# Performance work log

Measured on AMD Instinct MI355X. Metric: run time of the kernel, lower is better.

The kernel has to match this reference:

```python
import jax, jax.numpy as jnp
import numpy as np
from jax import lax

WAY = 20
EPS = 1e-10
CE_EPS = 1e-7
BN_EPS = 1e-3


def _conv_block(x, k, b, g, be):
    # conv 3x3 SAME -> batchnorm (batch stats, training mode) -> relu -> maxpool 2x2
    x = lax.conv_general_dilated(x, k, (1, 1), 'SAME',
                                 dimension_numbers=('NHWC', 'HWIO', 'NHWC')) + b
    m = x.mean((0, 1, 2))
    v = x.var((0, 1, 2))
    x = (x - m) * lax.rsqrt(v + BN_EPS) * g + be
    x = jax.nn.relu(x)
    x = lax.reduce_window(x, -jnp.inf, lax.max, (1, 2, 2, 1), (1, 2, 2, 1), 'VALID')
    return x


def _embed(x, cps):
    for (k, b, g, be) in cps:
        x = _conv_block(x, k, b, g, be)
    return x.reshape(x.shape[0], -1)  # [B, 1600]


def _lstm(seq, Wx, Wh, b):
    # seq: [batch, time, feat] -> [batch, time, hidden]
    B = seq.shape[0]
    H = Wh.shape[0]
    def step(carry, xt):
        h, c = carry
        z = xt @ Wx + h @ Wh + b
        i, f, g, o = jnp.split(z, 4, axis=-1)
        c = jax.nn.sigmoid(f) * c + jax.nn.sigmoid(i) * jnp.tanh(g)
        h = jax.nn.sigmoid(o) * jnp.tanh(c)
        return (h, c), h
    init = (jnp.zeros((B, H), seq.dtype), jnp.zeros((B, H), seq.dtype))
    _, hs = lax.scan(step, init, jnp.swapaxes(seq, 0, 1))
    return jnp.swapaxes(hs, 0, 1)


def _bilstm(seq, fk, fr, fb, bk, br, bb):
    fwd = _lstm(seq, fk, fr, fb)
    bwd = _lstm(seq[:, ::-1], bk, br, bb)[:, ::-1]
    return jnp.concatenate([fwd, bwd], axis=-1)


def setup_inputs() -> dict:
    key = jax.random.key(0)
    ks = jax.random.split(key, 12)
    B, S, Q, H, W, C = 32, 20, 5, 84, 84, 3
    inp = {
        'x_support': jax.random.normal(ks[0], (B, S, H, W, C), jnp.float32),
        'y_support': jax.random.randint(ks[1], (B, S), 0, WAY, jnp.int32),
        'x_query': jax.random.normal(ks[2], (B, Q, H, W, C), jnp.float32),
        'y_query': jax.random.randint(ks[3], (B, Q), 0, WAY, jnp.int32),
        'k1': jax.random.normal(ks[4], (3, 3, 3, 64), jnp.float32) * 0.05,
        'b1': jnp.zeros((64,), jnp.float32), 'g1': jnp.ones((64,), jnp.float32), 'be1': jnp.zeros((64,), jnp.float32),
        'k2': jax.random.normal(ks[5], (3, 3, 64, 64), jnp.float32) * 0.05,
        'b2': jnp.zeros((64,), jnp.float32), 'g2': jnp.ones((64,), jnp.float32), 'be2': jnp.zeros((64,), jnp.float32),
        'k3': jax.random.normal(ks[6], (3, 3, 64, 64), jnp.float32) * 0.05,
        'b3': jnp.zeros((64,), jnp.float32), 'g3': jnp.ones((64,), jnp.float32), 'be3': jnp.zeros((64,), jnp.float32),
        'k4': jax.random.normal(ks[7], (3, 3, 64, 64), jnp.float32) * 0.05,
        'b4': jnp.zeros((64,), jnp.float32), 'g4': jnp.ones((64,), jnp.float32), 'be4': jnp.zeros((64,), jnp.float32),
        'fk': jax.random.normal(ks[8], (1600, 128), jnp.float32) * 0.05,
        'fr': jax.random.normal(ks[9], (32, 128), jnp.float32) * 0.05,
        'fb': jnp.zeros((128,), jnp.float32),
        'bk': jax.random.normal(ks[10], (1600, 128), jnp.float32) * 0.05,
        'br': jax.random.normal(ks[11], (32, 128), jnp.float32) * 0.05,
        'bb': jnp.zeros((128,), jnp.float32),
    }
    return inp


def reference(x_support, y_support, x_query, y_query,
              k1, b1, g1, be1, k2, b2, g2, be2, k3, b3, g3, be3, k4, b4, g4, be4,
              fk, fr, fb, bk, br, bb):
    cps = ((k1, b1, g1, be1), (k2, b2, g2, be2), (k3, b3, g3, be3), (k4, b4, g4, be4))
    B, S = x_support.shape[:2]
    Q = x_query.shape[1]

    # per-sample embedding (BN stats per slice, matching the original per-i g() calls)
    sup_emb = jax.vmap(lambda xs: _embed(xs, cps), in_axes=1)(x_support)  # [S, B, F]
    qry_emb = jax.vmap(lambda xs: _embed(xs, cps), in_axes=1)(x_query)    # [Q, B, F]

    # stack [support..., query] -> [S+1, B, F]; Keras LSTM treats axis0 as batch, axis1(=B) as time
    seqs = jnp.concatenate([jnp.broadcast_to(sup_emb[None], (Q,) + sup_emb.shape),
                            qry_emb[:, None]], axis=1)  # [Q, S+1, B, F]
    outs = jax.vmap(lambda s: _bilstm(s, fk, fr, fb, bk, br, bb))(seqs)  # [Q, S+1, B, 64]

    sup = outs[:, :-1]   # [Q, S, B, 64]
    qry = outs[:, -1]    # [Q, B, 64]

    # cosine distance: only the support vector is normalized (faithful to original)
    mag = lax.rsqrt(jnp.maximum(jnp.sum(sup * sup, axis=-1), EPS))  # [Q, S, B]
    dot = jnp.einsum('qbd,qsbd->qsb', qry, sup)                      # [Q, S, B]
    sim = jax.nn.softmax(jnp.transpose(dot * mag, (0, 2, 1)), axis=-1)  # [Q, B, S]

    y_sup_oh = jax.nn.one_hot(y_support, WAY, dtype=jnp.float32)    # [B, S, WAY]
    preds = jnp.einsum('qbs,bsw->qbw', sim, y_sup_oh)                # [Q, B, WAY]

    y_q_oh = jnp.transpose(jax.nn.one_hot(y_query, WAY, dtype=jnp.float32), (1, 0, 2))  # [Q, B, WAY]
    ce = -jnp.sum(y_q_oh * jnp.log(jnp.clip(preds, CE_EPS, 1.0 - CE_EPS)), axis=-1)      # [Q, B]
    ce_out = jnp.sum(ce, axis=0) / Q  # [B]

    pred_lbl = jnp.argmax(preds, axis=-1).astype(jnp.int32)          # [Q, B]
    eq = (pred_lbl == jnp.transpose(y_query).astype(jnp.int32)).astype(jnp.float32)
    acc = jnp.sum(jnp.mean(eq, axis=1)) / Q  # scalar
    return (ce_out, acc)
```

## Files before the change

kernel.cpp:

```cpp
#include <hip/hip_runtime.h>
#include <hip/hip_bf16.h>


#define NG 25
#define NI 32

typedef _Float16 half8v __attribute__((ext_vector_type(8)));
typedef __attribute__((ext_vector_type(4))) float float4v;

__device__ __forceinline__ unsigned short f2h(float f) {
    _Float16 h = (_Float16)f;
    union { _Float16 h; unsigned short u; } cv; cv.h = h;
    return cv.u;
}
__device__ __forceinline__ float h2f(unsigned short u) {
    union { unsigned short u; _Float16 h; } cv; cv.u = u;
    return (float)cv.h;
}

__device__ __forceinline__ float fsigm(float x) {
    return __builtin_amdgcn_rcpf(1.f + exp2f(-1.44269504f * x));
}
__device__ __forceinline__ float ftanh(float x) {
    return 1.f - 2.f * __builtin_amdgcn_rcpf(1.f + exp2f(2.88539008f * x));
}

__global__ __launch_bounds__(256)
void wcvt_kernel(const float* __restrict__ wk, unsigned short* __restrict__ w16t) {
    int tap = blockIdx.x;
    for (int e = threadIdx.x; e < 4096; e += 256) {
        int co = e >> 6, ci = e & 63;
        w16t[(size_t)tap * 4096 + e] = f2h(wk[(size_t)tap * 4096 + ci * 64 + co]);
    }
}

__global__ __launch_bounds__(256)
void conv3m_kernel(const float* __restrict__ xs, const float* __restrict__ xq,
                   const float* __restrict__ wk, unsigned short* __restrict__ pool1h,
                   float* __restrict__ part, int g0) {
    __shared__ _Float16 sIn[10][304];
    __shared__ float sred[4][2][64];
    int gi = blockIdx.x;
    int gl = gi >> 5, i = gi & 31;
    int g = g0 + gl;
    int band = blockIdx.y;
    const float* base = (g < 20) ? xs + (size_t)(i * 20 + g) * (84 * 84 * 3)
                                 : xq + (size_t)(i * 5 + (g - 20)) * (84 * 84 * 3);
    int r0 = band * 8;
    for (int p = threadIdx.x; p < 10 * 152; p += 256) {
        int rr = p / 152, ep = (p - rr * 152) * 2;
        int r = r0 - 1 + rr;
        float v0 = 0.f, v1 = 0.f;
        if (ep < 294 && (unsigned)r < 84u) {
            int col0 = ep / 3 - 1, ci0 = ep - (ep / 3) * 3;
            if ((unsigned)col0 < 84u) v0 = base[((size_t)r * 84 + col0) * 3 + ci0];
            int e1 = ep + 1;
            if (e1 < 294) {
                int col1 = e1 / 3 - 1, ci1 = e1 - (e1 / 3) * 3;
                if ((unsigned)col1 < 84u) v1 = base[((size_t)r * 84 + col1) * 3 + ci1];
            }
        }
        unsigned int pk = (unsigned int)f2h(v0) | ((unsigned int)f2h(v1) << 16);
        ((unsigned int*)&sIn[rr][0])[p - rr * 152] = pk;
    }
    int lane = threadIdx.x & 63;
    int wv = threadIdx.x >> 6;
    int gq = lane >> 4;
    int l16 = lane & 15;
    int rowo[8], eo[8]; bool kv[8];
    #pragma unroll
    for (int j = 0; j < 8; ++j) {
        int k = 8 * gq + j;
        kv[j] = (k < 27);
        int kk = kv[j] ? k : 0;
        int kh = kk / 9; int rem = kk - kh * 9; int kw = rem / 3; int ci = rem - kw * 3;
        rowo[j] = kv[j] ? kh : 0;
        eo[j] = kw * 3 + ci;
    }
    half8v bfr[4];
    #pragma unroll
    for (int ct = 0; ct < 4; ++ct)
        #pragma unroll
        for (int j = 0; j < 8; ++j) {
            int k = 8 * gq + j;
            float w = (k < 27) ? wk[(size_t)k * 64 + ct * 16 + l16] : 0.f;
            bfr[ct][j] = (_Float16)w;
        }
    __syncthreads();

    bool rowv = (r0 + 2 * wv) < 84;
    int prow = band * 4 + wv;
    int sr = 2 * wv;
    float sA[4] = {0.f, 0.f, 0.f, 0.f}, sB[4] = {0.f, 0.f, 0.f, 0.f};

    #pragma unroll 1
    for (int tile = 0; tile < 6; ++tile) {
        int c0 = tile * 16;
        int w = c0 + l16;
        int eoff[8];
        #pragma unroll
        for (int j = 0; j < 8; ++j) eoff[j] = kv[j] ? (w * 3 + eo[j]) : 294;
        float4v acc0[4], acc1[4];
        #pragma unroll
        for (int ct = 0; ct < 4; ++ct) {
            acc0[ct] = (float4v){0.f, 0.f, 0.f, 0.f};
            acc1[ct] = (float4v){0.f, 0.f, 0.f, 0.f};
        }
        #pragma unroll
        for (int rs = 0; rs < 2; ++rs) {
            half8v af;
            #pragma unroll
            for (int j = 0; j < 8; ++j)
                af[j] = sIn[sr + rs + rowo[j]][eoff[j]];
            if (rs == 0) {
                #pragma unroll
                for (int ct = 0; ct < 4; ++ct)
                    acc0[ct] = __builtin_amdgcn_mfma_f32_16x16x32_f16(af, bfr[ct], acc0[ct], 0, 0, 0);
            } else {
                #pragma unroll
                for (int ct = 0; ct < 4; ++ct)
                    acc1[ct] = __builtin_amdgcn_mfma_f32_16x16x32_f16(af, bfr[ct], acc1[ct], 0, 0, 0);
            }
        }
        #pragma unroll
        for (int ct = 0; ct < 4; ++ct) {
            #pragma unroll
            for (int r = 0; r < 4; ++r) {
                float a0 = acc0[ct][r], a1 = acc1[ct][r];
                sA[ct] += a0 + a1;
                sB[ct] = fmaf(a0, a0, fmaf(a1, a1, sB[ct]));
            }
            if (rowv) {
                float m01 = fmaxf(fmaxf(acc0[ct][0], acc0[ct][1]),
                                  fmaxf(acc1[ct][0], acc1[ct][1]));
                float m23 = fmaxf(fmaxf(acc0[ct][2], acc0[ct][3]),
                                  fmaxf(acc1[ct][2], acc1[ct][3]));
                int pc0 = (c0 + gq * 4) >> 1;
                size_t rowbase = (((size_t)gi * 42 + prow) * 42) * 64 + ct * 16 + l16;
                if (pc0 < 42)     pool1h[rowbase + (size_t)pc0 * 64] = f2h(m01);
                if (pc0 + 1 < 42) pool1h[rowbase + (size_t)(pc0 + 1) * 64] = f2h(m23);
            }
        }
    }
    #pragma unroll
    for (int ct = 0; ct < 4; ++ct) {
        float s = sA[ct], q = sB[ct];
        s += __shfl_xor(s, 16); s += __shfl_xor(s, 32);
        q += __shfl_xor(q, 16); q += __shfl_xor(q, 32);
        if (gq == 0) { sred[wv][0][ct * 16 + l16] = s; sred[wv][1][ct * 16 + l16] = q; }
    }
    __syncthreads();
    if (threadIdx.x < 64) {
        int co = threadIdx.x;
        float s = sred[0][0][co] + sred[1][0][co] + sred[2][0][co] + sred[3][0][co];
        float q = sred[0][1][co] + sred[1][1][co] + sred[2][1][co] + sred[3][1][co];
        size_t pr = (size_t)blockIdx.y * gridDim.x + blockIdx.x;
        part[pr * 128 + co] = s;
        part[pr * 128 + 64 + co] = q;
    }
}

template<int D>
__global__ __launch_bounds__(256)
void conv64m_kernel(const unsigned short* __restrict__ act16,
                    const unsigned short* __restrict__ w16t,
                    float* __restrict__ poolout, float* __restrict__ part) {
    constexpr int nCT = (D + 15) / 16;
    constexpr int PD = D / 2;
    __shared__ __align__(16) char smem[64 * 72 * 2 * 2];
    unsigned short (*Albs)[72] = (unsigned short(*)[72])smem;
    unsigned short (*Blbs)[72] = (unsigned short(*)[72])(smem + 64 * 72 * 2);
    float (*lds2)[68] = (float(*)[68])smem;
    __shared__ float redst[2][4][64];

    int gi = blockIdx.x;
    int rt = blockIdx.y / nCT, ctile = blockIdx.y % nCT;
    int r0 = rt * 8, c0 = ctile * 16;
    const unsigned short* in = act16 + (size_t)gi * D * D * 64;

    int lane = threadIdx.x & 63;
    int wv = threadIdx.x >> 6;
    int pw = wv * 16;

    int spos = threadIdx.x >> 2;
    int scig = threadIdx.x & 3;
    int str = spos >> 4, stc = spos & 15;
    int sh = r0 + str, swc = c0 + stc;
    bool pval = (sh < D) && (swc < D);

    float4v acc[4];
    #pragma unroll
    for (int ct = 0; ct < 4; ++ct) acc[ct] = (float4v){0.f, 0.f, 0.f, 0.f};

    #pragma unroll 1
    for (int tap = 0; tap < 9; ++tap) {
        int kh = tap / 3, kw = tap - kh * 3;
        int hi = sh + kh - 1, wi = swc + kw - 1;
        uint4 av0 = {0,0,0,0}, av1 = {0,0,0,0};
        if (pval && (unsigned)hi < (unsigned)D && (unsigned)wi < (unsigned)D) {
            const uint4* src = (const uint4*)(in + ((size_t)hi * D + wi) * 64 + scig * 16);
            av0 = src[0]; av1 = src[1];
        }
        const uint4* wsrc = (const uint4*)(w16t + ((size_t)tap * 64 + spos) * 64 + scig * 16);
        uint4 bv0 = wsrc[0], bv1 = wsrc[1];
        __syncthreads();
        *(uint4*)&Albs[spos][scig * 16]     = av0;
        *(uint4*)&Albs[spos][scig * 16 + 8] = av1;
        *(uint4*)&Blbs[spos][scig * 16]     = bv0;
        *(uint4*)&Blbs[spos][scig * 16 + 8] = bv1;
        __syncthreads();
        #pragma unroll
        for (int ks = 0; ks < 2; ++ks) {
            half8v afrag = *(const half8v*)&Albs[pw + (lane & 15)][ks * 32 + (lane >> 4) * 8];
            #pragma unroll
            for (int ct = 0; ct < 4; ++ct) {
                half8v bfrag = *(const half8v*)&Blbs[ct * 16 + (lane & 15)][ks * 32 + (lane >> 4) * 8];
                acc[ct] = __builtin_amdgcn_mfma_f32_16x16x32_f16(afrag, bfrag, acc[ct], 0, 0, 0);
            }
        }
    }

    __syncthreads();
    #pragma unroll
    for (int ct = 0; ct < 4; ++ct) {
        #pragma unroll
        for (int r = 0; r < 4; ++r) {
            int pos = pw + (lane >> 4) * 4 + r;
            int co = ct * 16 + (lane & 15);
            lds2[pos][co] = acc[ct][r];
        }
    }
    __syncthreads();
    {
        int co = threadIdx.x & 63;
        int p4 = threadIdx.x >> 6;
        float s = 0.f, s2 = 0.f;
        #pragma unroll
        for (int p = 0; p < 16; ++p) {
            float a = lds2[p4 * 16 + p][co];
            s += a; s2 = fmaf(a, a, s2);
        }
        redst[0][p4][co] = s; redst[1][p4][co] = s2;
    }
    __syncthreads();
    if ((threadIdx.x >> 6) == 0) {
        int co = threadIdx.x & 63;
        float ts  = redst[0][0][co] + redst[0][1][co] + redst[0][2][co] + redst[0][3][co];
        float ts2 = redst[1][0][co] + redst[1][1][co] + redst[1][2][co] + redst[1][3][co];
        size_t prow = (size_t)blockIdx.y * gridDim.x + blockIdx.x;
        part[prow * 128 + co] = ts;
        part[prow * 128 + 64 + co] = ts2;
    }
    for (int o = threadIdx.x; o < 4 * 8 * 64; o += 256) {
        int cell = o >> 6, ch = o & 63;
        int pr = cell >> 3, pc = cell & 7;
        int p00 = (2 * pr) * 16 + 2 * pc;
        float m = fmaxf(fmaxf(lds2[p00][ch], lds2[p00 + 1][ch]),
                        fmaxf(lds2[p00 + 16][ch], lds2[p00 + 17][ch]));
        int gpr = rt * 4 + pr, gpc = ctile * 8 + pc;
        if (gpr < PD && gpc < PD)
            poolout[(((size_t)gi * PD + gpr) * PD + gpc) * 64 + ch] = m;
    }
}

__global__ __launch_bounds__(256)
void bn_finalize_kernel(const float* __restrict__ part,
                        const float* __restrict__ gamma,
                        const float* __restrict__ beta,
                        float* __restrict__ bnp, float invN, int nby, int gridx) {
    int g = blockIdx.x;
    int c = blockIdx.y;
    int nrows = nby * 32;
    float s = 0.f, s2 = 0.f;
    for (int rr = threadIdx.x; rr < nrows; rr += 256) {
        int by = rr >> 5, i = rr & 31;
        size_t row = (size_t)by * gridx + g * 32 + i;
        s  += part[row * 128 + c];
        s2 += part[row * 128 + 64 + c];
    }
    __shared__ float red[2][256];
    red[0][threadIdx.x] = s; red[1][threadIdx.x] = s2;
    __syncthreads();
    #pragma unroll
    for (int o = 128; o > 0; o >>= 1) {
        if (threadIdx.x < o) {
            red[0][threadIdx.x] += red[0][threadIdx.x + o];
            red[1][threadIdx.x] += red[1][threadIdx.x + o];
        }
        __syncthreads();
    }
    if (threadIdx.x == 0) {
        s = red[0][0]; s2 = red[1][0];
        float mean = s * invN;
        float var  = s2 * invN - mean * mean;
        float sc = gamma[c] * rsqrtf(var + 1e-3f);
        bnp[g * 128 + c] = sc;
        bnp[g * 128 + 64 + c] = beta[c] - sc * mean;
    }
}

__global__ __launch_bounds__(256)
void bnapplyh_ip_kernel(unsigned short* __restrict__ buf, const float* __restrict__ bnp,
                        int PP, int total) {
    int v = blockIdx.x * 256 + threadIdx.x;
    if (v >= total) return;
    int c4 = (v & 15) * 4;
    int pos = v >> 4;
    int gi = pos / PP;
    int gl = gi >> 5;
    float4 sc = *(const float4*)&bnp[gl * 128 + c4];
    float4 sh = *(const float4*)&bnp[gl * 128 + 64 + c4];
    ushort4 x = *(const ushort4*)&buf[(size_t)pos * 64 + c4];
    ushort4 o;
    o.x = f2h(fmaxf(0.f, fmaf(sc.x, h2f(x.x), sh.x)));
    o.y = f2h(fmaxf(0.f, fmaf(sc.y, h2f(x.y), sh.y)));
    o.z = f2h(fmaxf(0.f, fmaf(sc.z, h2f(x.z), sh.z)));
    o.w = f2h(fmaxf(0.f, fmaf(sc.w, h2f(x.w), sh.w)));
    *(ushort4*)&buf[(size_t)pos * 64 + c4] = o;
}

__global__ __launch_bounds__(256)
void bnapplyh_kernel(const float* __restrict__ buf, const float* __restrict__ bnp,
                     unsigned short* __restrict__ outh, int PP, int total) {
    int v = blockIdx.x * 256 + threadIdx.x;
    if (v >= total) return;
    int c4 = (v & 15) * 4;
    int pos = v >> 4;
    int gi = pos / PP;
    int gl = gi >> 5;
    float4 sc = *(const float4*)&bnp[gl * 128 + c4];
    float4 sh = *(const float4*)&bnp[gl * 128 + 64 + c4];
    float4 x = *(const float4*)&buf[(size_t)pos * 64 + c4];
    ushort4 o;
    o.x = f2h(fmaxf(0.f, fmaf(sc.x, x.x, sh.x)));
    o.y = f2h(fmaxf(0.f, fmaf(sc.y, x.y, sh.y)));
    o.z = f2h(fmaxf(0.f, fmaf(sc.z, x.z, sh.z)));
    o.w = f2h(fmaxf(0.f, fmaf(sc.w, x.w, sh.w)));
    *(ushort4*)&outh[(size_t)pos * 64 + c4] = o;
}

__global__ __launch_bounds__(256)
void bnapply_kernel(float* __restrict__ buf, const float* __restrict__ bnp,
                    int PP, int total) {
    int v = blockIdx.x * 256 + threadIdx.x;
    if (v >= total) return;
    int c4 = (v & 15) * 4;
    int pos = v >> 4;
    int gi = pos / PP;
    int gl = gi >> 5;
    float4 sc = *(const float4*)&bnp[gl * 128 + c4];
    float4 sh = *(const float4*)&bnp[gl * 128 + 64 + c4];
    float4 x = *(const float4*)&buf[(size_t)pos * 64 + c4];
    float4 o;
    o.x = fmaxf(0.f, fmaf(sc.x, x.x, sh.x));
    o.y = fmaxf(0.f, fmaf(sc.y, x.y, sh.y));
    o.z = fmaxf(0.f, fmaf(sc.z, x.z, sh.z));
    o.w = fmaxf(0.f, fmaf(sc.w, x.w, sh.w));
    *(float4*)&buf[(size_t)pos * 64 + c4] = o;
}

__global__ __launch_bounds__(256)
void xw2_kernel(const float* __restrict__ emb, const float* __restrict__ fk,
                const float* __restrict__ bk, float* __restrict__ xwpart) {
    __shared__ float se[16][200];
    int rt = blockIdx.x;
    int kb = blockIdx.y;
    for (int idx = threadIdx.x; idx < 16 * 200; idx += 256) {
        int r = idx / 200, kk = idx - (idx / 200) * 200;
        se[r][kk] = emb[(size_t)(rt * 16 + r) * 1600 + kb * 200 + kk];
    }
    __syncthreads();
    int j = threadIdx.x & 127;
    int half = threadIdx.x >> 7;
    const float* Wm = half ? bk : fk;
    float acc[16];
    #pragma unroll
    for (int r = 0; r < 16; ++r) acc[r] = 0.f;
    for (int kk = 0; kk < 200; ++kk) {
        float w = Wm[(size_t)(kb * 200 + kk) * 128 + j];
        #pragma unroll
        for (int r = 0; r < 16; ++r) acc[r] = fmaf(se[r][kk], w, acc[r]);
    }
    #pragma unroll
    for (int r = 0; r < 16; ++r)
        xwpart[((size_t)kb * 800 + rt * 16 + r) * 256 + half * 128 + j] = acc[r];
}

__global__ __launch_bounds__(256)
void xwred_kernel(const float* __restrict__ xwpart, float* __restrict__ xwf,
                  float* __restrict__ xwb) {
    int gi = blockIdx.x;
    int c = threadIdx.x;
    float s = 0.f;
    #pragma unroll
    for (int kb = 0; kb < 8; ++kb)
        s += xwpart[((size_t)kb * 800 + gi) * 256 + c];
    if (c < 128) xwf[(size_t)gi * 128 + c] = s;
    else         xwb[(size_t)gi * 128 + (c - 128)] = s;
}

__global__ __launch_bounds__(64, 1)
void lstm_kernel(const float* __restrict__ xwf, const float* __restrict__ xwb,
                 const float* __restrict__ fr, const float* __restrict__ fb,
                 const float* __restrict__ br, const float* __restrict__ bb,
                 float* __restrict__ Hs) {
    int g = blockIdx.x;
    int dir = blockIdx.y;
    int j = threadIdx.x;
    const float* xw = dir ? xwb : xwf;
    const float* Wr = dir ? br : fr;
    const float* bv = dir ? bb : fb;
    float frA[32], frB[32];
    #pragma unroll
    for (int k = 0; k < 32; ++k) {
        frA[k] = Wr[k * 128 + j];
        frB[k] = Wr[k * 128 + 64 + j];
    }
    float bA = bv[j], bB = bv[64 + j];
    float xA[32], xB[32];
    #pragma unroll
    for (int st = 0; st < 32; ++st) {
        int t = dir ? (31 - st) : st;
        xA[st] = xw[((size_t)g * NI + t) * 128 + j];
        xB[st] = xw[((size_t)g * NI + t) * 128 + 64 + j];
    }
    float h = 0.f, c = 0.f;
    #pragma unroll
    for (int st = 0; st < 32; ++st) {
        int t = dir ? (31 - st) : st;
        float a0 = xA[st] + bA, a1 = 0.f, a2 = 0.f, a3 = 0.f;
        float b0 = xB[st] + bB, b1 = 0.f, b2 = 0.f, b3 = 0.f;
        #pragma unroll
        for (int kk = 0; kk < 8; ++kk) {
            float h0 = __shfl(h, kk);
            float h1 = __shfl(h, kk + 8);
            float h2 = __shfl(h, kk + 16);
            float h3 = __shfl(h, kk + 24);
            a0 = fmaf(h0, frA[kk], a0);      b0 = fmaf(h0, frB[kk], b0);
            a1 = fmaf(h1, frA[kk + 8], a1);  b1 = fmaf(h1, frB[kk + 8], b1);
            a2 = fmaf(h2, frA[kk + 16], a2); b2 = fmaf(h2, frB[kk + 16], b2);
            a3 = fmaf(h3, frA[kk + 24], a3); b3 = fmaf(h3, frB[kk + 24], b3);
        }
        float accA = (a0 + a1) + (a2 + a3);
        float accB = (b0 + b1) + (b2 + b3);
        float ig = accA;
        float gg = accB;
        float fg = __shfl(accA, (j & 31) + 32);
        float og = __shfl(accB, (j & 31) + 32);
        float cn = fsigm(fg) * c + fsigm(ig) * ftanh(gg);
        float hn = fsigm(og) * ftanh(cn);
        if (j < 32) {
            c = cn; h = hn;
            Hs[((size_t)g * NI + t) * 64 + dir * 32 + j] = hn;
        }
    }
}

__global__ __launch_bounds__(64, 1)
void sim_kernel(const float* __restrict__ Hs, const int* __restrict__ ysup,
                const int* __restrict__ yq, float* __restrict__ ceb,
                float* __restrict__ eqb) {
    int q = blockIdx.x;
    int i = blockIdx.y;
    int lane = threadIdx.x;
    float qv = Hs[((size_t)(20 + q) * NI + i) * 64 + lane];
    float ls[20];
    for (int s = 0; s < 20; ++s) {
        float sv = Hs[((size_t)s * NI + i) * 64 + lane];
        float d = qv * sv;
        float m = sv * sv;
        #pragma unroll
        for (int o = 32; o > 0; o >>= 1) {
            d += __shfl_xor(d, o);
            m += __shfl_xor(m, o);
        }
        ls[s] = d * rsqrtf(fmaxf(m, 1e-10f));
    }
    if (lane == 0) {
        float mx = -1e30f;
        for (int s = 0; s < 20; ++s) mx = fmaxf(mx, ls[s]);
        float sum = 0.f, sim[20];
        for (int s = 0; s < 20; ++s) { sim[s] = expf(ls[s] - mx); sum += sim[s]; }
        float inv = 1.f / sum;
        float preds[20];
        for (int w = 0; w < 20; ++w) preds[w] = 0.f;
        for (int s = 0; s < 20; ++s) preds[ysup[i * 20 + s]] += sim[s] * inv;
        int y = yq[i * 5 + q];
        float pv = fminf(fmaxf(preds[y], 1e-7f), 1.f - 1e-7f);
        ceb[q * NI + i] = -logf(pv);
        int am = 0; float bm = preds[0];
        for (int w = 1; w < 20; ++w) if (preds[w] > bm) { bm = preds[w]; am = w; }
        eqb[q * NI + i] = (am == y) ? 1.f : 0.f;
    }
}

__global__ __launch_bounds__(64, 1)
void final_kernel(const float* __restrict__ ceb, const float* __restrict__ eqb,
                  float* __restrict__ out) {
    int lane = threadIdx.x;
    float e = 0.f;
    if (lane < 32) {
        float ce = 0.f;
        for (int q = 0; q < 5; ++q) { ce += ceb[q * NI + lane]; e += eqb[q * NI + lane]; }
        out[lane] = ce * 0.2f;
    }
    #pragma unroll
    for (int o = 32; o > 0; o >>= 1) e += __shfl_xor(e, o);
    if (lane == 0) out[32] = e / 160.f;
}

__global__ void sentinel_kernel(float* out) {
    if (threadIdx.x < 33) out[threadIdx.x] = -777.25f;
}

extern "C" void kernel_launch(void* const* d_in, const int* in_sizes, int n_in,
                              void* d_out, int out_size, void* d_ws, size_t ws_size,
                              hipStream_t stream) {
    const float* xs   = (const float*)d_in[0];
    const int*   ysup = (const int*)  d_in[1];
    const float* xq   = (const float*)d_in[2];
    const int*   yq   = (const int*)  d_in[3];
    const float* k[4]  = { (const float*)d_in[4],  (const float*)d_in[8],
                           (const float*)d_in[12], (const float*)d_in[16] };
    const float* ga[4] = { (const float*)d_in[6],  (const float*)d_in[10],
                           (const float*)d_in[14], (const float*)d_in[18] };
    const float* be[4] = { (const float*)d_in[7],  (const float*)d_in[11],
                           (const float*)d_in[15], (const float*)d_in[19] };
    const float* fk = (const float*)d_in[20];
    const float* fr = (const float*)d_in[21];
    const float* fb = (const float*)d_in[22];
    const float* bk = (const float*)d_in[23];
    const float* br = (const float*)d_in[24];
    const float* bb = (const float*)d_in[25];
    float* out = (float*)d_out;

    const size_t P1   = (size_t)NI * 42 * 42 * 64;
    const size_t P2   = (size_t)NI * 21 * 21 * 64;
    const size_t P3   = (size_t)NI * 10 * 10 * 64;
    const size_t PERG = P1 / 2 + (P2 + P3) * 3 / 2 + 21u * 32 * 128 + 128;
    const size_t FIXED = 1280000 + 2 * 102400 + 51200 + 320 + 73728 + 1638400;

    const int cands[14] = {25, 20, 18, 16, 14, 12, 10, 8, 6, 5, 4, 3, 2, 1};
    int C = 0;
    for (int t = 0; t < 14; ++t) {
        int c = cands[t];
        if (((size_t)c * PERG + FIXED) * sizeof(float) <= ws_size) { C = c; break; }
    }
    if (C == 0) {
        sentinel_kernel<<<1, 64, 0, stream>>>(out);
        return;
    }

    float* W = (float*)d_ws;
    size_t off = 0;
    unsigned short* pool1h = (unsigned short*)(W + off); off += (size_t)C * P1 / 2;
    float* pool2 = W + off; off += (size_t)C * P2;
    float* pool3 = W + off; off += (size_t)C * P3;
    unsigned short* pool2h = (unsigned short*)(W + off); off += (size_t)C * P2 / 2;
    unsigned short* pool3h = (unsigned short*)(W + off); off += (size_t)C * P3 / 2;
    float* emb   = W + off; off += 1280000;
    float* part  = W + off; off += 21u * (size_t)C * 32 * 128;
    float* bnp   = W + off; off += (size_t)C * 128;
    unsigned short* w16t = (unsigned short*)(W + off); off += 73728;
    float* xwpart = W + off; off += 1638400;
    float* xwf   = W + off; off += 102400;
    float* xwb   = W + off; off += 102400;
    float* Hs    = W + off; off += 51200;
    float* ceb   = W + off; off += 160;
    float* eqb   = W + off; off += 160;

    for (int l = 1; l < 4; ++l)
        wcvt_kernel<<<9, 256, 0, stream>>>(k[l], w16t + (size_t)l * 9 * 4096);

    for (int g0 = 0; g0 < NG; g0 += C) {
        int ngc = (NG - g0 < C) ? (NG - g0) : C;
        int gx = ngc * 32;

        conv3m_kernel<<<dim3(gx, 11), 256, 0, stream>>>(xs, xq, k[0], pool1h, part, g0);
        bn_finalize_kernel<<<dim3(ngc, 64), 256, 0, stream>>>(part, ga[0], be[0], bnp, 1.f / (32.f * 84 * 84), 11, gx);
        bnapplyh_ip_kernel<<<(gx * 42 * 42 * 16 + 255) / 256, 256, 0, stream>>>(pool1h, bnp, 42 * 42, gx * 42 * 42 * 16);

        conv64m_kernel<42><<<dim3(gx, 18), 256, 0, stream>>>(pool1h, w16t + 9 * 4096, pool2, part);
        bn_finalize_kernel<<<dim3(ngc, 64), 256, 0, stream>>>(part, ga[1], be[1], bnp, 1.f / (32.f * 42 * 42), 18, gx);
        bnapplyh_kernel<<<(gx * 21 * 21 * 16 + 255) / 256, 256, 0, stream>>>(pool2, bnp, pool2h, 21 * 21, gx * 21 * 21 * 16);

        conv64m_kernel<21><<<dim3(gx, 6), 256, 0, stream>>>(pool2h, w16t + 2 * 9 * 4096, pool3, part);
        bn_finalize_kernel<<<dim3(ngc, 64), 256, 0, stream>>>(part, ga[2], be[2], bnp, 1.f / (32.f * 21 * 21), 6, gx);
        bnapplyh_kernel<<<(gx * 100 * 16 + 255) / 256, 256, 0, stream>>>(pool3, bnp, pool3h, 100, gx * 100 * 16);

        conv64m_kernel<10><<<dim3(gx, 2), 256, 0, stream>>>(pool3h, w16t + 3 * 9 * 4096, emb + (size_t)g0 * 32 * 1600, part);
        bn_finalize_kernel<<<dim3(ngc, 64), 256, 0, stream>>>(part, ga[3], be[3], bnp, 1.f / (32.f * 100), 2, gx);
        bnapply_kernel<<<(gx * 25 * 16 + 255) / 256, 256, 0, stream>>>(emb + (size_t)g0 * 32 * 1600, bnp, 25, gx * 25 * 16);
    }

    xw2_kernel<<<dim3(50, 8), 256, 0, stream>>>(emb, fk, bk, xwpart);
    xwred_kernel<<<800, 256, 0, stream>>>(xwpart, xwf, xwb);

    lstm_kernel<<<dim3(NG, 2), 64, 0, stream>>>(xwf, xwb, fr, fb, br, bb, Hs);
    sim_kernel<<<dim3(5, 32), 64, 0, stream>>>(Hs, ysup, yq, ceb, eqb);
    final_kernel<<<1, 64, 0, stream>>>(ceb, eqb, out);
}
```

Baseline: 567.7 us.

## Stage halo tile once in LDS, keep weights in registers, write fp16 pooled output

The 3x3 conv64 kernel now loads a 10x18 halo tile of input into LDS once and holds all 9 taps of weights in registers per wave. This replaces the per-tap global reload with two barriers each time, and computes an 8-row by 16-col tile with each wave owning 16 output channels. BN statistics and 2x2 max-pool are done directly from the MFMA accumulators with shuffles, with no LDS round trip. Pooled outputs for layers 2 and 3 are written as fp16 and normalized in place, which drops the fp32 intermediate buffers and the separate conversion kernel. The trade-off is higher register pressure from 72 weight fragments per thread, an added launch-bounds occupancy hint, and fp16 rounding of pre-BN pooled values.

After: 1.646 ms. 2.9x slower.

```diff
diff --git a/kernel.cpp b/kernel.cpp
--- a/kernel.cpp
+++ b/kernel.cpp
@@ -24,6 +24,9 @@
 __device__ __forceinline__ float ftanh(float x) {
     return 1.f - 2.f * __builtin_amdgcn_rcpf(1.f + exp2f(2.88539008f * x));
 }
+
+__device__ __forceinline__ void pstore(float* p, size_t off, float v) { p[off] = v; }
+__device__ __forceinline__ void pstore(unsigned short* p, size_t off, float v) { p[off] = f2h(v); }
 
 __global__ __launch_bounds__(256)
 void wcvt_kernel(const float* __restrict__ wk, unsigned short* __restrict__ w16t) {
@@ -160,19 +163,14 @@
     }
 }
 
-template<int D>
-__global__ __launch_bounds__(256)
+template<int D, typename OutT>
+__global__ __launch_bounds__(256, 3)
 void conv64m_kernel(const unsigned short* __restrict__ act16,
                     const unsigned short* __restrict__ w16t,
-                    float* __restrict__ poolout, float* __restrict__ part) {
+                    OutT* __restrict__ poolout, float* __restrict__ part) {
     constexpr int nCT = (D + 15) / 16;
     constexpr int PD = D / 2;
-    __shared__ __align__(16) char smem[64 * 72 * 2 * 2];
-    unsigned short (*Albs)[72] = (unsigned short(*)[72])smem;
-    unsigned short (*Blbs)[72] = (unsigned short(*)[72])(smem + 64 * 72 * 2);
-    float (*lds2)[68] = (float(*)[68])smem;
-    __shared__ float redst[2][4][64];
-
+    __shared__ __align__(16) unsigned short sH[10 * 18 * 72];
     int gi = blockIdx.x;
     int rt = blockIdx.y / nCT, ctile = blockIdx.y % nCT;
     int r0 = rt * 8, c0 = ctile * 16;
@@ -180,86 +178,77 @@
 
     int lane = threadIdx.x & 63;
     int wv = threadIdx.x >> 6;
-    int pw = wv * 16;
-
-    int spos = threadIdx.x >> 2;
-    int scig = threadIdx.x & 3;
-    int str = spos >> 4, stc = spos & 15;
-    int sh = r0 + str, swc = c0 + stc;
-    bool pval = (sh < D) && (swc < D);
-
-    float4v acc[4];
-    #pragma unroll
-    for (int ct = 0; ct < 4; ++ct) acc[ct] = (float4v){0.f, 0.f, 0.f, 0.f};
-
-    #pragma unroll 1
+    int gq = lane >> 4;
+    int l16 = lane & 15;
+
+    half8v bfr[9][2];
+    #pragma unroll
+    for (int tap = 0; tap < 9; ++tap)
+        #pragma unroll
+        for (int ks = 0; ks < 2; ++ks)
+            bfr[tap][ks] = *(const half8v*)&w16t[((size_t)tap * 64 + wv * 16 + l16) * 64 + ks * 32 + gq * 8];
+
+    for (int s = threadIdx.x; s < 10 * 18 * 8; s += 256) {
+        int row = s / 144, rem = s - row * 144;
+        int col = rem >> 3, q = rem & 7;
+        int h = r0 + row - 1, w = c0 + col - 1;
+        uint4 v = {0, 0, 0, 0};
+        if ((unsigned)h < (unsigned)D && (unsigned)w < (unsigned)D)
+            v = *(const uint4*)&in[((size_t)h * D + w) * 64 + q * 8];
+        *(uint4*)&sH[row * 1296 + col * 72 + q * 8] = v;
+    }
+    __syncthreads();
+
+    float4v acc[8];
+    #pragma unroll
+    for (int m = 0; m < 8; ++m) acc[m] = (float4v){0.f, 0.f, 0.f, 0.f};
+
+    int abase = (l16) * 72 + gq * 8;
+    #pragma unroll
     for (int tap = 0; tap < 9; ++tap) {
-        int kh = tap / 3, kw = tap - kh * 3;
-        int hi = sh + kh - 1, wi = swc + kw - 1;
-        uint4 av0 = {0,0,0,0}, av1 = {0,0,0,0};
-        if (pval && (unsigned)hi < (unsigned)D && (unsigned)wi < (unsigned)D) {
-            const uint4* src = (const uint4*)(in + ((size_t)hi * D + wi) * 64 + scig * 16);
-            av0 = src[0]; av1 = src[1];
-        }
-        const uint4* wsrc = (const uint4*)(w16t + ((size_t)tap * 64 + spos) * 64 + scig * 16);
-        uint4 bv0 = wsrc[0], bv1 = wsrc[1];
-        __syncthreads();
-        *(uint4*)&Albs[spos][scig * 16]     = av0;
-        *(uint4*)&Albs[spos][scig * 16 + 8] = av1;
-        *(uint4*)&Blbs[spos][scig * 16]     = bv0;
-        *(uint4*)&Blbs[spos][scig * 16 + 8] = bv1;
-        __syncthreads();
+        constexpr int dummy = 0; (void)dummy;
+        const int kh = tap / 3, kw = tap - (tap / 3) * 3;
         #pragma unroll
         for (int ks = 0; ks < 2; ++ks) {
-            half8v afrag = *(const half8v*)&Albs[pw + (lane & 15)][ks * 32 + (lane >> 4) * 8];
             #pragma unroll
-            for (int ct = 0; ct < 4; ++ct) {
-                half8v bfrag = *(const half8v*)&Blbs[ct * 16 + (lane & 15)][ks * 32 + (lane >> 4) * 8];
-                acc[ct] = __builtin_amdgcn_mfma_f32_16x16x32_f16(afrag, bfrag, acc[ct], 0, 0, 0);
+            for (int m = 0; m < 8; ++m) {
+                half8v af = *(const half8v*)&sH[(m + kh) * 1296 + kw * 72 + ks * 32 + abase];
+                acc[m] = __builtin_amdgcn_mfma_f32_16x16x32_f16(af, bfr[tap][ks], acc[m], 0, 0, 0);
             }
         }
     }
 
-    __syncthreads();
-    #pragma unroll
-    for (int ct = 0; ct < 4; ++ct) {
-        #pragma unroll
-        for (int r = 0; r < 4; ++r) {
-            int pos = pw + (lane >> 4) * 4 + r;
-            int co = ct * 16 + (lane & 15);
-            lds2[pos][co] = acc[ct][r];
-        }
-    }
-    __syncthreads();
     {
-        int co = threadIdx.x & 63;
-        int p4 = threadIdx.x >> 6;
         float s = 0.f, s2 = 0.f;
         #pragma unroll
-        for (int p = 0; p < 16; ++p) {
-            float a = lds2[p4 * 16 + p][co];
-            s += a; s2 = fmaf(a, a, s2);
-        }
-        redst[0][p4][co] = s; redst[1][p4][co] = s2;
-    }
-    __syncthreads();
-    if ((threadIdx.x >> 6) == 0) {
-        int co = threadIdx.x & 63;
-        float ts  = redst[0][0][co] + redst[0][1][co] + redst[0][2][co] + redst[0][3][co];
-        float ts2 = redst[1][0][co] + redst[1][1][co] + redst[1][2][co] + redst[1][3][co];
-        size_t prow = (size_t)blockIdx.y * gridDim.x + blockIdx.x;
-        part[prow * 128 + co] = ts;
-        part[prow * 128 + 64 + co] = ts2;
-    }
-    for (int o = threadIdx.x; o < 4 * 8 * 64; o += 256) {
-        int cell = o >> 6, ch = o & 63;
-        int pr = cell >> 3, pc = cell & 7;
-        int p00 = (2 * pr) * 16 + 2 * pc;
-        float m = fmaxf(fmaxf(lds2[p00][ch], lds2[p00 + 1][ch]),
-                        fmaxf(lds2[p00 + 16][ch], lds2[p00 + 17][ch]));
-        int gpr = rt * 4 + pr, gpc = ctile * 8 + pc;
-        if (gpr < PD && gpc < PD)
-            poolout[(((size_t)gi * PD + gpr) * PD + gpc) * 64 + ch] = m;
+        for (int m = 0; m < 8; ++m)
+            #pragma unroll
+            for (int r = 0; r < 4; ++r) {
+                float a = acc[m][r];
+                s += a; s2 = fmaf(a, a, s2);
+            }
+        s += __shfl_xor(s, 16); s += __shfl_xor(s, 32);
+        s2 += __shfl_xor(s2, 16); s2 += __shfl_xor(s2, 32);
+        if (gq == 0) {
+            size_t prow = (size_t)blockIdx.y * gridDim.x + blockIdx.x;
+            part[prow * 128 + wv * 16 + l16] = s;
+            part[prow * 128 + 64 + wv * 16 + l16] = s2;
+        }
+    }
+    int ch = wv * 16 + l16;
+    #pragma unroll
+    for (int p = 0; p < 4; ++p) {
+        float m01 = fmaxf(fmaxf(acc[2 * p][0], acc[2 * p][1]),
+                          fmaxf(acc[2 * p + 1][0], acc[2 * p + 1][1]));
+        float m23 = fmaxf(fmaxf(acc[2 * p][2], acc[2 * p][3]),
+                          fmaxf(acc[2 * p + 1][2], acc[2 * p + 1][3]));
+        int gpr = rt * 4 + p;
+        int gpc0 = ctile * 8 + gq * 2;
+        if (gpr < PD) {
+            size_t rb = (((size_t)gi * PD + gpr) * PD) * 64 + ch;
+            if (gpc0 < PD)     pstore(poolout, rb + (size_t)gpc0 * 64, m01);
+            if (gpc0 + 1 < PD) pstore(poolout, rb + (size_t)(gpc0 + 1) * 64, m23);
+        }
     }
 }
 
@@ -317,26 +306,6 @@
     o.z = f2h(fmaxf(0.f, fmaf(sc.z, h2f(x.z), sh.z)));
     o.w = f2h(fmaxf(0.f, fmaf(sc.w, h2f(x.w), sh.w)));
     *(ushort4*)&buf[(size_t)pos * 64 + c4] = o;
-}
-
-__global__ __launch_bounds__(256)
-void bnapplyh_kernel(const float* __restrict__ buf, const float* __restrict__ bnp,
-                     unsigned short* __restrict__ outh, int PP, int total) {
-    int v = blockIdx.x * 256 + threadIdx.x;
-    if (v >= total) return;
-    int c4 = (v & 15) * 4;
-    int pos = v >> 4;
-    int gi = pos / PP;
-    int gl = gi >> 5;
-    float4 sc = *(const float4*)&bnp[gl * 128 + c4];
-    float4 sh = *(const float4*)&bnp[gl * 128 + 64 + c4];
-    float4 x = *(const float4*)&buf[(size_t)pos * 64 + c4];
-    ushort4 o;
-    o.x = f2h(fmaxf(0.f, fmaf(sc.x, x.x, sh.x)));
-    o.y = f2h(fmaxf(0.f, fmaf(sc.y, x.y, sh.y)));
-    o.z = f2h(fmaxf(0.f, fmaf(sc.z, x.z, sh.z)));
-    o.w = f2h(fmaxf(0.f, fmaf(sc.w, x.w, sh.w)));
-    *(ushort4*)&outh[(size_t)pos * 64 + c4] = o;
 }
 
 __global__ __launch_bounds__(256)
@@ -537,7 +506,7 @@
     const size_t P1   = (size_t)NI * 42 * 42 * 64;
     const size_t P2   = (size_t)NI * 21 * 21 * 64;
     const size_t P3   = (size_t)NI * 10 * 10 * 64;
-    const size_t PERG = P1 / 2 + (P2 + P3) * 3 / 2 + 21u * 32 * 128 + 128;
+    const size_t PERG = (P1 + P2 + P3) / 2 + 21u * 32 * 128 + 128;
     const size_t FIXED = 1280000 + 2 * 102400 + 51200 + 320 + 73728 + 1638400;
 
     const int cands[14] = {25, 20, 18, 16, 14, 12, 10, 8, 6, 5, 4, 3, 2, 1};
@@ -554,8 +523,6 @@
     float* W = (float*)d_ws;
     size_t off = 0;
     unsigned short* pool1h = (unsigned short*)(W + off); off += (size_t)C * P1 / 2;
-    float* pool2 = W + off; off += (size_t)C * P2;
-    float* pool3 = W + off; off += (size_t)C * P3;
     unsigned short* pool2h = (unsigned short*)(W + off); off += (size_t)C * P2 / 2;
     unsigned short* pool3h = (unsigned short*)(W + off); off += (size_t)C * P3 / 2;
     float* emb   = W + off; off += 1280000;
@@ -580,15 +547,15 @@
         bn_finalize_kernel<<<dim3(ngc, 64), 256, 0, stream>>>(part, ga[0], be[0], bnp, 1.f / (32.f * 84 * 84), 11, gx);
         bnapplyh_ip_kernel<<<(gx * 42 * 42 * 16 + 255) / 256, 256, 0, stream>>>(pool1h, bnp, 42 * 42, gx * 42 * 42 * 16);
 
-        conv64m_kernel<42><<<dim3(gx, 18), 256, 0, stream>>>(pool1h, w16t + 9 * 4096, pool2, part);
+        conv64m_kernel<42, unsigned short><<<dim3(gx, 18), 256, 0, stream>>>(pool1h, w16t + 9 * 4096, pool2h, part);
         bn_finalize_kernel<<<dim3(ngc, 64), 256, 0, stream>>>(part, ga[1], be[1], bnp, 1.f / (32.f * 42 * 42), 18, gx);
-        bnapplyh_kernel<<<(gx * 21 * 21 * 16 + 255) / 256, 256, 0, stream>>>(pool2, bnp, pool2h, 21 * 21, gx * 21 * 21 * 16);
-
-        conv64m_kernel<21><<<dim3(gx, 6), 256, 0, stream>>>(pool2h, w16t + 2 * 9 * 4096, pool3, part);
+        bnapplyh_ip_kernel<<<(gx * 21 * 21 * 16 + 255) / 256, 256, 0, stream>>>(pool2h, bnp, 21 * 21, gx * 21 * 21 * 16);
+
+        conv64m_kernel<21, unsigned short><<<dim3(gx, 6), 256, 0, stream>>>(pool2h, w16t + 2 * 9 * 4096, pool3h, part);
         bn_finalize_kernel<<<dim3(ngc, 64), 256, 0, stream>>>(part, ga[2], be[2], bnp, 1.f / (32.f * 21 * 21), 6, gx);
-        bnapplyh_kernel<<<(gx * 100 * 16 + 255) / 256, 256, 0, stream>>>(pool3, bnp, pool3h, 100, gx * 100 * 16);
-
-        conv64m_kernel<10><<<dim3(gx, 2), 256, 0, stream>>>(pool3h, w16t + 3 * 9 * 4096, emb + (size_t)g0 * 32 * 1600, part);
+        bnapplyh_ip_kernel<<<(gx * 100 * 16 + 255) / 256, 256, 0, stream>>>(pool3h, bnp, 100, gx * 100 * 16);
+
+        conv64m_kernel<10, float><<<dim3(gx, 2), 256, 0, stream>>>(pool3h, w16t + 3 * 9 * 4096, emb + (size_t)g0 * 32 * 1600, part);
         bn_finalize_kernel<<<dim3(ngc, 64), 256, 0, stream>>>(part, ga[3], be[3], bnp, 1.f / (32.f * 100), 2, gx);
         bnapply_kernel<<<(gx * 25 * 16 + 255) / 256, 256, 0, stream>>>(emb + (size_t)g0 * 32 * 1600, bnp, 25, gx * 25 * 16);
     }
```
